# Optimization experiments

Measured on AMD Instinct MI355X. Metric: run time of the kernel, lower is better.

The kernel has to match this reference:

```python
import jax, jax.numpy as jnp
import numpy as np

B, C, H, W = 4, 64, 64, 64
RC, RS = 8, 4  # channel reduction, spatial reduction
CR = C // RC
KS = 2 * RS - 1  # 7


def _conv(x, w, b, stride, pad):
    y = jax.lax.conv_general_dilated(
        x, w, (stride, stride), [(pad, pad), (pad, pad)],
        dimension_numbers=('NCHW', 'OIHW', 'NCHW'))
    return y + b[None, :, None, None]


def setup_inputs() -> dict:
    key = jax.random.key(0)
    ks = jax.random.split(key, 13)

    def w_init(k, shape):
        fan_in = shape[1] * shape[2] * shape[3]
        return jax.random.normal(k, shape, jnp.float32) / jnp.sqrt(fan_in)

    x = jax.random.normal(ks[0], (B, C, H, W), jnp.float32)
    return {
        'x': x,
        'w1': w_init(ks[1], (CR, C, 1, 1)), 'b1': jnp.zeros((CR,), jnp.float32),
        'w2': w_init(ks[2], (CR, C, 1, 1)), 'b2': jnp.zeros((CR,), jnp.float32),
        'w3': w_init(ks[3], (C, C, 1, 1)),  'b3': jnp.zeros((C,), jnp.float32),
        'w4': w_init(ks[4], (C, C, KS, KS)), 'b4': jnp.zeros((C,), jnp.float32),
        'w5': w_init(ks[5], (C, C, KS, KS)), 'b5': jnp.zeros((C,), jnp.float32),
        'w6': w_init(ks[6], (C, C, 1, 1)),  'b6': jnp.zeros((C,), jnp.float32),
    }


def reference(x, w1, b1, w2, b2, w3, b3, w4, b4, w5, b5, w6, b6):
    gamma = 1.0
    x_ori = x
    b, c, h, w = x.shape
    n = h * w

    # ---- Block 1: spatial self-attention (SAGAN-style), N x N scores ----
    f = _conv(x, w1, b1, 1, 0).reshape(b, CR, n)   # [B, C/8, N]
    g = _conv(x, w2, b2, 1, 0).reshape(b, CR, n)   # [B, C/8, N]
    hh = _conv(x, w3, b3, 1, 0).reshape(b, c, n)   # [B, C, N]
    s = jnp.einsum('bci,bcj->bij', f, g)           # [B, N, N] = f^T g
    beta = jax.nn.softmax(s, axis=1)               # softmax over dim 1 (as in torch)
    o = jnp.einsum('bcn,bnm->bcm', hh, beta)       # [B, C, N]
    x2 = o.reshape(b, c, h, w)

    # ---- Block 2: channel attention over strided-conv features, C x C scores ----
    hp, wp = h // RS, w // RS
    npix = hp * wp
    f2 = _conv(x2, w4, b4, RS, RS - 1).reshape(b, c, npix)  # [B, C, N']
    g2 = _conv(x2, w5, b5, RS, RS - 1).reshape(b, c, npix)  # [B, C, N']
    h2 = _conv(x2, w6, b6, 1, 0).reshape(b, c, n)           # [B, C, N]
    s2 = jnp.einsum('bcn,bdn->bcd', f2, g2)                 # [B, C, C] = f g^T
    beta2 = jax.nn.softmax(s2, axis=1)
    # o[b,d,n] = sum_c h2[b,c,n] * beta2[b,c,d]
    o2 = jnp.einsum('bcn,bcd->bdn', h2, beta2).reshape(b, c, h, w)

    return gamma * o2 + x_ori
```

## Files before the change

kernel.cpp:

```cpp
#include <hip/hip_runtime.h>
#include <math.h>

#define BB 4
#define CC 64
#define CRR 8
#define NN 4096

typedef __attribute__((ext_vector_type(8))) short bf16x8;
typedef __attribute__((ext_vector_type(4))) float f32x4;

__device__ inline float bf2f(ushort u) {
    union { uint i; float f; } v; v.i = (uint)u << 16; return v.f;
}
__device__ inline ushort f2bf(float f) {
    uint u = __builtin_bit_cast(uint, f);
    u = (u + 0x7FFFu + ((u >> 16) & 1u)) >> 16;
    return (ushort)u;
}
__device__ inline uint bfpack2(float a, float b) {
    uint ua = __builtin_bit_cast(uint, a);
    uint ub = __builtin_bit_cast(uint, b);
    ua = (ua + 0x7FFFu + ((ua >> 16) & 1u)) >> 16;
    ub = (ub + 0x7FFFu + ((ub >> 16) & 1u)) & 0xFFFF0000u;
    return ua | ub;
}
__device__ inline uint pkrtz(float a, float b) {
    return __builtin_amdgcn_perm(__builtin_bit_cast(uint, b),
                                 __builtin_bit_cast(uint, a), 0x07060302u);
}
__device__ inline float fexp2(float x) {
#if __has_builtin(__builtin_amdgcn_exp2f)
    return __builtin_amdgcn_exp2f(x);
#else
    float r; asm("v_exp_f32 %0, %1" : "=v"(r) : "v"(x)); return r;
#endif
}

#define X2P_B 313600

__global__ __launch_bounds__(256) void produce_fgh(
    const float* __restrict__ x,
    const float* __restrict__ w1, const float* __restrict__ b1,
    const float* __restrict__ w2, const float* __restrict__ b2,
    const float* __restrict__ w3, const float* __restrict__ b3,
    ushort* __restrict__ fT, ushort* __restrict__ gT, ushort* __restrict__ hhb)
{
    const float LOG2E = 1.4426950408889634f;
    int t = threadIdx.x;
    int b = blockIdx.x & 3;
    int n = ((blockIdx.x >> 2) << 6) + (t & 63);
    int og = __builtin_amdgcn_readfirstlane(t >> 6);

    const float* xb = x + ((size_t)b << 18) + n;
    float xv[64];
#pragma unroll
    for (int c = 0; c < 64; ++c) xv[c] = xb[(size_t)c << 12];

    if (og == 0) {
        ushort fo[8], go[8];
#pragma unroll
        for (int k = 0; k < 8; ++k) {
            float a1 = b1[k], a2 = b2[k];
#pragma unroll
            for (int c = 0; c < 64; ++c) {
                a1 = fmaf(w1[k * 64 + c], xv[c], a1);
                a2 = fmaf(w2[k * 64 + c], xv[c], a2);
            }
            fo[k] = f2bf(a1 * LOG2E); go[k] = f2bf(a2);
        }
        uint4 fq = make_uint4((uint)fo[0] | ((uint)fo[1] << 16),
                              (uint)fo[2] | ((uint)fo[3] << 16),
                              (uint)fo[4] | ((uint)fo[5] << 16),
                              (uint)fo[6] | ((uint)fo[7] << 16));
        uint4 gq = make_uint4((uint)go[0] | ((uint)go[1] << 16),
                              (uint)go[2] | ((uint)go[3] << 16),
                              (uint)go[4] | ((uint)go[5] << 16),
                              (uint)go[6] | ((uint)go[7] << 16));
        *(uint4*)&fT[((size_t)b << 15) + (size_t)n * 8] = fq;
        *(uint4*)&gT[((size_t)b << 15) + (size_t)n * 8] = gq;
#pragma unroll
        for (int k = 0; k < 4; ++k) {
            float a = b3[k];
#pragma unroll
            for (int c = 0; c < 64; ++c) a = fmaf(w3[k * 64 + c], xv[c], a);
            hhb[((size_t)b << 18) + ((size_t)k << 12) + n] = f2bf(a);
        }
    } else {
        int c0 = og * 20 - 16;
#pragma unroll
        for (int k = 0; k < 20; ++k) {
            float a = b3[c0 + k];
#pragma unroll
            for (int c = 0; c < 64; ++c) a = fmaf(w3[(c0 + k) * 64 + c], xv[c], a);
            hhb[((size_t)b << 18) + ((size_t)(c0 + k) << 12) + n] = f2bf(a);
        }
    }
}

__global__ __launch_bounds__(256) void wtz_kernel(
    const float* __restrict__ w4, const float* __restrict__ w5,
    const float* __restrict__ w6,
    ushort* __restrict__ Wt, ushort* __restrict__ w6b, ushort* __restrict__ x2p)
{
    int bid = blockIdx.x;
    int t = threadIdx.x;
    if (bid < 128) {
        int conv = bid >> 6, co = bid & 63;
        const float* W = conv ? w5 : w4;
        for (int i = t; i < 3136; i += 256) {
            int ci = i / 49, kk = i - ci * 49;
            Wt[(((size_t)(conv * 64 + co)) * 49 + kk) * 64 + ci] = f2bf(W[co * 3136 + i]);
        }
    } else if (bid == 128) {
#pragma unroll
        for (int k = 0; k < 16; ++k) {
            int i = k * 256 + t;
            w6b[i] = f2bf(w6[i]);
        }
    } else {
        int gid = (bid - 129) * 256 + t;
        if (gid >= 4 * 804) return;
        int b = gid / 804;
        int i = gid - b * 804;
        int py, px;
        if (i < 210) { py = i / 70; px = i - py * 70; }
        else if (i < 420) { int j = i - 210; int r = j / 70; py = 67 + r; px = j - r * 70; }
        else { int j = i - 420; int r = j / 6; py = 3 + r; int c = j - r * 6; px = c < 3 ? c : 64 + c; }
        ushort* p = x2p + (size_t)b * X2P_B + (size_t)(py * 70 + px) * 64;
        uint4 z = make_uint4(0, 0, 0, 0);
#pragma unroll
        for (int k = 0; k < 8; ++k) *(uint4*)(p + k * 8) = z;
    }
}

__global__ __launch_bounds__(1024) void attn_kernel(
    const ushort* __restrict__ fT, const ushort* __restrict__ gT,
    const ushort* __restrict__ hhb, const ushort* __restrict__ w6b,
    const float* __restrict__ b6,
    ushort* __restrict__ x2p, ushort* __restrict__ h2b)
{
    __shared__ __align__(16) char smem[98304];
    ushort* hhT = (ushort*)smem;
    ushort* PstB = (ushort*)(smem + 65536);
    float* Acc = (float*)smem;
    float* Lq  = (float*)(smem + 69632);
    ushort* x2s = (ushort*)(smem + 70656);

    int t = threadIdx.x;
    int q = t >> 8, tq = t & 255;
    int l = t & 63;
    int wq = tq >> 6;
    int w16 = t >> 6;
    int ml = l & 15, g = l >> 4;
    int b = blockIdx.x & 3;
    int mt = blockIdx.x >> 2;
    int m0 = mt << 6;
    int col = m0 + wq * 16 + ml;

    const ushort* fTb = fT + ((size_t)b << 15) + (size_t)q * 8192;
    const ushort* gTb = gT + ((size_t)b << 15);
    const ushort* hhB = hhb + ((size_t)b << 18) + (q << 10);

    const bf16x8 z8 = {0, 0, 0, 0, 0, 0, 0, 0};
    const f32x4 z4 = {0.f, 0.f, 0.f, 0.f};

    bf16x8 gfrag = *(const bf16x8*)(gTb + (size_t)col * 8);
    if (g != 0) gfrag = z8;

    int sc = tq >> 2, sp = tq & 3;
    const ushort* hrowBase = hhB + (size_t)sc * 4096 + sp * 16;
    int hdst = q * 8192 + sp * 1024 + sc * 8;

    uint4 h0 = *(const uint4*)(hrowBase);
    uint4 h1 = *(const uint4*)(hrowBase + 8);
    *(uint4*)&hhT[hdst] = h0;
    *(uint4*)&hhT[hdst + 512] = h1;
    bf16x8 afc[4];
#pragma unroll
    for (int s = 0; s < 4; ++s)
        afc[s] = *(const bf16x8*)(fTb + (size_t)(16 * s + ml) * 8);

    f32x4 acc[4] = {z4, z4, z4, z4};
    float rsum = 0.f;
    int swz = (ml & 7) << 4;
    char* pbase = (char*)PstB + w16 * 2048;
    __syncthreads();

    for (int nt = 0; nt < 16; ++nt) {
        int buf = nt & 1;
        bf16x8 afn[4];
        if (nt < 15) {
            int n0 = (nt + 1) << 6;
            h0 = *(const uint4*)(hrowBase + n0);
            h1 = *(const uint4*)(hrowBase + n0 + 8);
#pragma unroll
            for (int s = 0; s < 4; ++s)
                afn[s] = *(const bf16x8*)(fTb + (size_t)(n0 + 16 * s + ml) * 8);
        }

        f32x4 Sv[4];
#pragma unroll
        for (int s = 0; s < 4; ++s)
            Sv[s] = __builtin_amdgcn_mfma_f32_16x16x32_bf16(afc[s], gfrag, z4, 0, 0, 0);

        uint plo[4], phi[4];
#pragma unroll
        for (int s = 0; s < 4; ++s) {
            float p0 = fexp2(Sv[s][0]);
            float p1 = fexp2(Sv[s][1]);
            float p2 = fexp2(Sv[s][2]);
            float p3 = fexp2(Sv[s][3]);
            rsum += (p0 + p1) + (p2 + p3);
            plo[s] = pkrtz(p0, p1);
            phi[s] = pkrtz(p2, p3);
        }

#pragma unroll
        for (int s = 0; s < 4; ++s) {
            uint off = (uint)((ml * 128 + 32 * s + 8 * g) ^ swz);
            *(uint2*)(pbase + off) = make_uint2(plo[s], phi[s]);
        }

#pragma unroll
        for (int kk = 0; kk < 2; ++kk) {
            uint off = (uint)((ml * 128 + 64 * kk + 16 * g) ^ swz);
            bf16x8 pf = *(const bf16x8*)(pbase + off);
#pragma unroll
            for (int ct = 0; ct < 4; ++ct) {
                bf16x8 hf = *(const bf16x8*)&hhT[q * 8192 + buf * 4096 + (kk * 4 + g) * 512 + (16 * ct + ml) * 8];
                acc[ct] = __builtin_amdgcn_mfma_f32_16x16x32_bf16(hf, pf, acc[ct], 0, 0, 0);
            }
        }

        if (nt < 15) {
            int nb = (nt + 1) & 1;
            *(uint4*)&hhT[hdst + nb * 4096] = h0;
            *(uint4*)&hhT[hdst + nb * 4096 + 512] = h1;
#pragma unroll
            for (int s = 0; s < 4; ++s) afc[s] = afn[s];
        }
        __syncthreads();
    }

    rsum += __shfl_xor(rsum, 16);
    rsum += __shfl_xor(rsum, 32);

    {
        float* arow = Acc + q * 4352 + (wq * 16 + ml) * 68;
#pragma unroll
        for (int ct = 0; ct < 4; ++ct)
            *(f32x4*)(arow + 16 * ct + 4 * g) = acc[ct];
        if (g == 0) Lq[q * 64 + wq * 16 + ml] = rsum;
    }
    __syncthreads();

    {
        int m = t >> 4, c0 = (t & 15) << 2;
        float Ltot = Lq[m] + Lq[64 + m] + Lq[128 + m] + Lq[192 + m];
        float rL = 1.f / Ltot;
        f32x4 v0 = *(const f32x4*)(Acc + 0 * 4352 + m * 68 + c0);
        f32x4 v1 = *(const f32x4*)(Acc + 1 * 4352 + m * 68 + c0);
        f32x4 v2 = *(const f32x4*)(Acc + 2 * 4352 + m * 68 + c0);
        f32x4 v3 = *(const f32x4*)(Acc + 3 * 4352 + m * 68 + c0);
        f32x4 v;
#pragma unroll
        for (int r = 0; r < 4; ++r)
            v[r] = ((v0[r] + v1[r]) + (v2[r] + v3[r])) * rL;
        uint2 pk = make_uint2(bfpack2(v[0], v[1]), bfpack2(v[2], v[3]));
        int px = m + 3, py = mt + 3;
        *(uint2*)(x2p + (size_t)b * X2P_B + (size_t)(py * 70 + px) * 64 + c0) = pk;
        *(uint2*)(x2s + m * 72 + c0) = pk;
    }
    __syncthreads();

    {
        int dt = w16 & 3, mq = w16 >> 2;
        f32x4 hacc = z4;
#pragma unroll
        for (int kk = 0; kk < 2; ++kk) {
            bf16x8 xf = *(const bf16x8*)(x2s + (mq * 16 + ml) * 72 + 32 * kk + 8 * g);
            bf16x8 wf = *(const bf16x8*)(w6b + (size_t)(16 * dt + ml) * 64 + 32 * kk + 8 * g);
            hacc = __builtin_amdgcn_mfma_f32_16x16x32_bf16(wf, xf, hacc, 0, 0, 0);
        }
        ushort* h2row = h2b + ((size_t)b << 18) + (m0 + mq * 16 + ml);
#pragma unroll
        for (int r = 0; r < 4; ++r) {
            int d = 16 * dt + 4 * g + r;
            h2row[(size_t)d << 12] = f2bf(hacc[r] + b6[d]);
        }
    }
}

__global__ __launch_bounds__(448) void conv7_kernel(
    const ushort* __restrict__ x2p, const ushort* __restrict__ Wt,
    const float* __restrict__ b4, const float* __restrict__ b5,
    float* __restrict__ f2, float* __restrict__ g2)
{
    __shared__ float red[7][512];
    int t = threadIdx.x;
    int l = t & 63, ky = t >> 6;
    int ml = l & 15, g = l >> 4;
    int bid = blockIdx.x;
    int bc = bid & 7;
    int sub = bid >> 3;
    int ct = sub & 3, oh = sub >> 2;
    int conv = bc & 1, b = bc >> 1;

    int co0 = ct * 16;
    const ushort* wb = Wt + (size_t)conv * 200704
                     + (size_t)(co0 + ml) * 3136 + (size_t)(ky * 7) * 64 + g * 8;
    const ushort* xbase = x2p + (size_t)b * X2P_B + g * 8;

    int pixoff[2];
#pragma unroll
    for (int s = 0; s < 2; ++s) {
        int opix = oh * 32 + s * 16 + ml;
        int oy = opix >> 4, ox = opix & 15;
        pixoff[s] = ((oy * 4 + ky) * 70 + ox * 4) * 64;
    }

    const f32x4 z4 = {0.f, 0.f, 0.f, 0.f};
    f32x4 acc[2] = {z4, z4};

#pragma unroll
    for (int kx = 0; kx < 7; ++kx) {
#pragma unroll
        for (int ci0 = 0; ci0 < 64; ci0 += 32) {
            bf16x8 av = *(const bf16x8*)(wb + kx * 64 + ci0);
#pragma unroll
            for (int s = 0; s < 2; ++s) {
                bf16x8 bv = *(const bf16x8*)(xbase + pixoff[s] + kx * 64 + ci0);
                acc[s] = __builtin_amdgcn_mfma_f32_16x16x32_bf16(av, bv, acc[s], 0, 0, 0);
            }
        }
    }

#pragma unroll
    for (int s = 0; s < 2; ++s)
#pragma unroll
        for (int r = 0; r < 4; ++r)
            red[ky][(4 * g + r) * 32 + s * 16 + ml] = acc[s][r];
    __syncthreads();

    const float* bias = conv ? b5 : b4;
    float* y = conv ? g2 : f2;
    for (int idx = t; idx < 512; idx += 448) {
        float s = red[0][idx];
        s += red[1][idx]; s += red[2][idx]; s += red[3][idx];
        s += red[4][idx]; s += red[5][idx]; s += red[6][idx];
        int co = co0 + (idx >> 5);
        int opix = oh * 32 + (idx & 31);
        y[((size_t)(b * 64 + co) << 8) + opix] = s + bias[co];
    }
}

__global__ __launch_bounds__(1024) void s2_softmax_kernel(
    const float* __restrict__ f2, const float* __restrict__ g2,
    float* __restrict__ beta2)
{
    __shared__ __align__(16) float g2t[4][64][68];
    __shared__ __align__(16) float s2f[64][68];
    __shared__ float red[6][64];
    int t = threadIdx.x;
    int b = blockIdx.x;
    int q = t >> 8, tq = t & 255;
    int nb = q * 64;

    {
        int n = tq & 63, c0 = tq >> 6;
#pragma unroll
        for (int k = 0; k < 16; ++k) {
            int cc = c0 * 16 + k;
            g2t[q][n][cc] = g2[((size_t)(b * 64 + cc) << 8) + nb + n];
        }
    }
    __syncthreads();

    int c = tq & 63, dq = tq >> 6, d0 = dq * 16;
    float acc[16];
#pragma unroll
    for (int k = 0; k < 16; ++k) acc[k] = 0.f;
    const float* frow = f2 + ((size_t)(b * 64 + c) << 8) + nb;
#pragma unroll 4
    for (int n = 0; n < 64; ++n) {
        float fv = frow[n];
#pragma unroll
        for (int jj = 0; jj < 4; ++jj) {
            float4 gv = *(const float4*)&g2t[q][n][d0 + jj * 4];
            acc[jj * 4 + 0] = fmaf(fv, gv.x, acc[jj * 4 + 0]);
            acc[jj * 4 + 1] = fmaf(fv, gv.y, acc[jj * 4 + 1]);
            acc[jj * 4 + 2] = fmaf(fv, gv.z, acc[jj * 4 + 2]);
            acc[jj * 4 + 3] = fmaf(fv, gv.w, acc[jj * 4 + 3]);
        }
    }
    __syncthreads();
    float* part = &g2t[0][0][0];
#pragma unroll
    for (int k = 0; k < 16; ++k) part[q * 4096 + c * 64 + d0 + k] = acc[k];
    __syncthreads();
    {
        int idx = t * 4;
        int cc = idx >> 6, dd = idx & 63;
        float4 s0 = *(const float4*)&part[cc * 64 + dd];
        float4 s1 = *(const float4*)&part[4096 + cc * 64 + dd];
        float4 s2v = *(const float4*)&part[8192 + cc * 64 + dd];
        float4 s3 = *(const float4*)&part[12288 + cc * 64 + dd];
        float4 s;
        s.x = (s0.x + s1.x) + (s2v.x + s3.x);
        s.y = (s0.y + s1.y) + (s2v.y + s3.y);
        s.z = (s0.z + s1.z) + (s2v.z + s3.z);
        s.w = (s0.w + s1.w) + (s2v.w + s3.w);
        *(float4*)&s2f[cc][dd] = s;
    }
    __syncthreads();
    if (t < 256) {
        int d = t & 63, cq = t >> 6;
        float mx = -3e38f;
#pragma unroll
        for (int k = 0; k < 16; ++k) mx = fmaxf(mx, s2f[cq * 16 + k][d]);
        red[cq][d] = mx;
    }
    __syncthreads();
    if (t < 64)
        red[4][t] = fmaxf(fmaxf(red[0][t], red[1][t]), fmaxf(red[2][t], red[3][t]));
    __syncthreads();
    if (t < 256) {
        int d = t & 63, cq = t >> 6;
        float mx = red[4][d];
        float s = 0.f;
#pragma unroll
        for (int k = 0; k < 16; ++k) s += __expf(s2f[cq * 16 + k][d] - mx);
        red[cq][d] = s;
    }
    __syncthreads();
    if (t < 64)
        red[5][t] = 1.f / ((red[0][t] + red[1][t]) + (red[2][t] + red[3][t]));
    __syncthreads();
    if (t < 256) {
        int d = t & 63, cq = t >> 6;
        float mx = red[4][d], r = red[5][d];
#pragma unroll
        for (int k = 0; k < 16; ++k) {
            int cc = cq * 16 + k;
            beta2[((size_t)b << 12) + cc * 64 + d] = __expf(s2f[cc][d] - mx) * r;
        }
    }
}

__global__ __launch_bounds__(256) void o2_residual_kernel(
    const ushort* __restrict__ h2b, const float* __restrict__ beta2,
    const float* __restrict__ x, float* __restrict__ out)
{
    __shared__ __align__(16) float b2s[64][64];
    __shared__ float h2s[64][65];
    int t = threadIdx.x;
    int b = blockIdx.x & 3;
    int n0 = (blockIdx.x >> 2) << 6;

    {
#pragma unroll
        for (int k = 0; k < 16; ++k) {
            int idx = k * 256 + t;
            b2s[idx >> 6][idx & 63] = beta2[((size_t)b << 12) + idx];
        }
        int n = t & 63; int c0 = t >> 6;
#pragma unroll
        for (int k = 0; k < 16; ++k) {
            int cc = c0 * 16 + k;
            h2s[cc][n] = bf2f(h2b[((size_t)(b * 64 + cc) << 12) + n0 + n]);
        }
    }
    __syncthreads();

    int n = t & 63, dg = t >> 6, d0 = dg * 16;
    float acc[16];
#pragma unroll
    for (int k = 0; k < 16; ++k) acc[k] = 0.f;

    for (int cc = 0; cc < 64; ++cc) {
        float hv = h2s[cc][n];
#pragma unroll
        for (int jj = 0; jj < 4; ++jj) {
            float4 bv = *reinterpret_cast<const float4*>(&b2s[cc][d0 + jj * 4]);
            acc[jj * 4 + 0] = fmaf(hv, bv.x, acc[jj * 4 + 0]);
            acc[jj * 4 + 1] = fmaf(hv, bv.y, acc[jj * 4 + 1]);
            acc[jj * 4 + 2] = fmaf(hv, bv.z, acc[jj * 4 + 2]);
            acc[jj * 4 + 3] = fmaf(hv, bv.w, acc[jj * 4 + 3]);
        }
    }
#pragma unroll
    for (int k = 0; k < 16; ++k) {
        int d = d0 + k;
        size_t o = ((size_t)(b * 64 + d) << 12) + n0 + n;
        out[o] = acc[k] + x[o];
    }
}

extern "C" void kernel_launch(void* const* d_in, const int* in_sizes, int n_in,
                              void* d_out, int out_size, void* d_ws, size_t ws_size,
                              hipStream_t stream)
{
    const float* x  = (const float*)d_in[0];
    const float* w1 = (const float*)d_in[1];
    const float* b1 = (const float*)d_in[2];
    const float* w2 = (const float*)d_in[3];
    const float* b2 = (const float*)d_in[4];
    const float* w3 = (const float*)d_in[5];
    const float* b3 = (const float*)d_in[6];
    const float* w4 = (const float*)d_in[7];
    const float* b4 = (const float*)d_in[8];
    const float* w5 = (const float*)d_in[9];
    const float* b5 = (const float*)d_in[10];
    const float* w6 = (const float*)d_in[11];
    const float* b6 = (const float*)d_in[12];
    float* out = (float*)d_out;

    ushort* u = (ushort*)d_ws;
    ushort* fT  = u;
    ushort* gT  = fT + 131072;
    ushort* hhb = gT + 131072;
    ushort* x2p = hhb + 1048576;
    ushort* h2b = x2p + 1254400;
    ushort* Wt  = h2b + 1048576;
    ushort* w6b = Wt + 401408;
    float* fr    = (float*)(w6b + 4096);
    float* f2    = fr;
    float* g2    = fr + 65536;
    float* beta2 = fr + 131072;

    produce_fgh<<<256, 256, 0, stream>>>(x, w1, b1, w2, b2, w3, b3, fT, gT, hhb);
    wtz_kernel<<<142, 256, 0, stream>>>(w4, w5, w6, Wt, w6b, x2p);
    attn_kernel<<<256, 1024, 0, stream>>>(fT, gT, hhb, w6b, b6, x2p, h2b);
    conv7_kernel<<<256, 448, 0, stream>>>(x2p, Wt, b4, b5, f2, g2);
    s2_softmax_kernel<<<BB, 1024, 0, stream>>>(f2, g2, beta2);
    o2_residual_kernel<<<256, 256, 0, stream>>>(h2b, beta2, x, out);
}
```

Before: 79.80 us.

## Split channel-score softmax across more blocks and use MFMA for output mix

The channel-attention score/softmax kernel used to run as 4 blocks of 1024 threads, one per batch. It now runs as 64 blocks, each computing four output columns, so more compute units take part. The output-mixing kernel moves from scalar FP32 FMAs to bf16 MFMA, splitting beta2 into high and low bf16 parts to keep accuracy. In exchange, f2 is read redundantly by every block and the split-bf16 product can lose some precision.

```diff
diff --git a/kernel.cpp b/kernel.cpp
--- a/kernel.cpp
+++ b/kernel.cpp
@@ -354,96 +354,80 @@
     }
 }
 
-__global__ __launch_bounds__(1024) void s2_softmax_kernel(
+__global__ __launch_bounds__(256) void s2_softmax_kernel(
     const float* __restrict__ f2, const float* __restrict__ g2,
     float* __restrict__ beta2)
 {
-    __shared__ __align__(16) float g2t[4][64][68];
-    __shared__ __align__(16) float s2f[64][68];
-    __shared__ float red[6][64];
+    __shared__ __align__(16) float g2t[256][8];
+    __shared__ __align__(16) float part[16][64][4];
+    __shared__ __align__(16) float s2f[64][4];
+    __shared__ float mx4[4], rs4[4];
     int t = threadIdx.x;
-    int b = blockIdx.x;
-    int q = t >> 8, tq = t & 255;
-    int nb = q * 64;
+    int b = blockIdx.x & 3;
+    int d0 = (blockIdx.x >> 2) << 2;
 
     {
-        int n = tq & 63, c0 = tq >> 6;
-#pragma unroll
-        for (int k = 0; k < 16; ++k) {
-            int cc = c0 * 16 + k;
-            g2t[q][n][cc] = g2[((size_t)(b * 64 + cc) << 8) + nb + n];
-        }
-    }
-    __syncthreads();
-
-    int c = tq & 63, dq = tq >> 6, d0 = dq * 16;
-    float acc[16];
-#pragma unroll
-    for (int k = 0; k < 16; ++k) acc[k] = 0.f;
-    const float* frow = f2 + ((size_t)(b * 64 + c) << 8) + nb;
+        int dd = t & 3, n0 = (t >> 2) << 2;
+        const float* gp = g2 + ((size_t)(b * 64 + d0 + dd) << 8) + n0;
+        float4 v = *(const float4*)gp;
+        g2t[n0 + 0][dd] = v.x; g2t[n0 + 1][dd] = v.y;
+        g2t[n0 + 2][dd] = v.z; g2t[n0 + 3][dd] = v.w;
+    }
+    __syncthreads();
+
+    int c0 = (t & 15) << 2, nq = t >> 4;
+    float acc[4][4];
+#pragma unroll
+    for (int i = 0; i < 4; ++i)
+#pragma unroll
+        for (int j = 0; j < 4; ++j) acc[i][j] = 0.f;
+    const float* fb = f2 + ((size_t)(b * 64) << 8);
 #pragma unroll 4
-    for (int n = 0; n < 64; ++n) {
-        float fv = frow[n];
-#pragma unroll
-        for (int jj = 0; jj < 4; ++jj) {
-            float4 gv = *(const float4*)&g2t[q][n][d0 + jj * 4];
-            acc[jj * 4 + 0] = fmaf(fv, gv.x, acc[jj * 4 + 0]);
-            acc[jj * 4 + 1] = fmaf(fv, gv.y, acc[jj * 4 + 1]);
-            acc[jj * 4 + 2] = fmaf(fv, gv.z, acc[jj * 4 + 2]);
-            acc[jj * 4 + 3] = fmaf(fv, gv.w, acc[jj * 4 + 3]);
-        }
-    }
-    __syncthreads();
-    float* part = &g2t[0][0][0];
-#pragma unroll
-    for (int k = 0; k < 16; ++k) part[q * 4096 + c * 64 + d0 + k] = acc[k];
+    for (int i = 0; i < 16; ++i) {
+        int n = (nq << 4) + ((i + nq) & 15);
+        float4 gv = *(const float4*)&g2t[n][0];
+        float fv0 = fb[(c0 + 0) * 256 + n];
+        float fv1 = fb[(c0 + 1) * 256 + n];
+        float fv2 = fb[(c0 + 2) * 256 + n];
+        float fv3 = fb[(c0 + 3) * 256 + n];
+        acc[0][0] = fmaf(fv0, gv.x, acc[0][0]); acc[0][1] = fmaf(fv0, gv.y, acc[0][1]);
+        acc[0][2] = fmaf(fv0, gv.z, acc[0][2]); acc[0][3] = fmaf(fv0, gv.w, acc[0][3]);
+        acc[1][0] = fmaf(fv1, gv.x, acc[1][0]); acc[1][1] = fmaf(fv1, gv.y, acc[1][1]);
+        acc[1][2] = fmaf(fv1, gv.z, acc[1][2]); acc[1][3] = fmaf(fv1, gv.w, acc[1][3]);
+        acc[2][0] = fmaf(fv2, gv.x, acc[2][0]); acc[2][1] = fmaf(fv2, gv.y, acc[2][1]);
+        acc[2][2] = fmaf(fv2, gv.z, acc[2][2]); acc[2][3] = fmaf(fv2, gv.w, acc[2][3]);
+        acc[3][0] = fmaf(fv3, gv.x, acc[3][0]); acc[3][1] = fmaf(fv3, gv.y, acc[3][1]);
+        acc[3][2] = fmaf(fv3, gv.z, acc[3][2]); acc[3][3] = fmaf(fv3, gv.w, acc[3][3]);
+    }
+#pragma unroll
+    for (int i = 0; i < 4; ++i)
+        *(float4*)&part[nq][c0 + i][0] =
+            make_float4(acc[i][0], acc[i][1], acc[i][2], acc[i][3]);
+    __syncthreads();
+
+    if (t < 64) {
+        int c = t;
+        float4 s = make_float4(0.f, 0.f, 0.f, 0.f);
+#pragma unroll
+        for (int q2 = 0; q2 < 16; ++q2) {
+            float4 v = *(const float4*)&part[q2][c][0];
+            s.x += v.x; s.y += v.y; s.z += v.z; s.w += v.w;
+        }
+        *(float4*)&s2f[c][0] = s;
+    }
+    __syncthreads();
+    if (t < 4) {
+        float mxv = s2f[0][t];
+        for (int c = 1; c < 64; ++c) mxv = fmaxf(mxv, s2f[c][t]);
+        float sm = 0.f;
+        for (int c = 0; c < 64; ++c) sm += __expf(s2f[c][t] - mxv);
+        mx4[t] = mxv; rs4[t] = 1.f / sm;
+    }
     __syncthreads();
     {
-        int idx = t * 4;
-        int cc = idx >> 6, dd = idx & 63;
-        float4 s0 = *(const float4*)&part[cc * 64 + dd];
-        float4 s1 = *(const float4*)&part[4096 + cc * 64 + dd];
-        float4 s2v = *(const float4*)&part[8192 + cc * 64 + dd];
-        float4 s3 = *(const float4*)&part[12288 + cc * 64 + dd];
-        float4 s;
-        s.x = (s0.x + s1.x) + (s2v.x + s3.x);
-        s.y = (s0.y + s1.y) + (s2v.y + s3.y);
-        s.z = (s0.z + s1.z) + (s2v.z + s3.z);
-        s.w = (s0.w + s1.w) + (s2v.w + s3.w);
-        *(float4*)&s2f[cc][dd] = s;
-    }
-    __syncthreads();
-    if (t < 256) {
-        int d = t & 63, cq = t >> 6;
-        float mx = -3e38f;
-#pragma unroll
-        for (int k = 0; k < 16; ++k) mx = fmaxf(mx, s2f[cq * 16 + k][d]);
-        red[cq][d] = mx;
-    }
-    __syncthreads();
-    if (t < 64)
-        red[4][t] = fmaxf(fmaxf(red[0][t], red[1][t]), fmaxf(red[2][t], red[3][t]));
-    __syncthreads();
-    if (t < 256) {
-        int d = t & 63, cq = t >> 6;
-        float mx = red[4][d];
-        float s = 0.f;
-#pragma unroll
-        for (int k = 0; k < 16; ++k) s += __expf(s2f[cq * 16 + k][d] - mx);
-        red[cq][d] = s;
-    }
-    __syncthreads();
-    if (t < 64)
-        red[5][t] = 1.f / ((red[0][t] + red[1][t]) + (red[2][t] + red[3][t]));
-    __syncthreads();
-    if (t < 256) {
-        int d = t & 63, cq = t >> 6;
-        float mx = red[4][d], r = red[5][d];
-#pragma unroll
-        for (int k = 0; k < 16; ++k) {
-            int cc = cq * 16 + k;
-            beta2[((size_t)b << 12) + cc * 64 + d] = __expf(s2f[cc][d] - mx) * r;
-        }
+        int c = t >> 2, dd = t & 3;
+        beta2[((size_t)b << 12) + c * 64 + d0 + dd] =
+            __expf(s2f[c][dd] - mx4[dd]) * rs4[dd];
     }
 }
 
@@ -451,49 +435,63 @@
     const ushort* __restrict__ h2b, const float* __restrict__ beta2,
     const float* __restrict__ x, float* __restrict__ out)
 {
-    __shared__ __align__(16) float b2s[64][64];
-    __shared__ float h2s[64][65];
+    __shared__ __align__(16) ushort bt[64][68];
+    __shared__ __align__(16) ushort btl[64][68];
+    __shared__ __align__(16) ushort hn[64][68];
     int t = threadIdx.x;
     int b = blockIdx.x & 3;
     int n0 = (blockIdx.x >> 2) << 6;
+    int l = t & 63, w = t >> 6;
+    int ml = l & 15, g = l >> 4;
 
     {
-#pragma unroll
-        for (int k = 0; k < 16; ++k) {
-            int idx = k * 256 + t;
-            b2s[idx >> 6][idx & 63] = beta2[((size_t)b << 12) + idx];
-        }
-        int n = t & 63; int c0 = t >> 6;
-#pragma unroll
-        for (int k = 0; k < 16; ++k) {
-            int cc = c0 * 16 + k;
-            h2s[cc][n] = bf2f(h2b[((size_t)(b * 64 + cc) << 12) + n0 + n]);
-        }
-    }
-    __syncthreads();
-
-    int n = t & 63, dg = t >> 6, d0 = dg * 16;
-    float acc[16];
-#pragma unroll
-    for (int k = 0; k < 16; ++k) acc[k] = 0.f;
-
-    for (int cc = 0; cc < 64; ++cc) {
-        float hv = h2s[cc][n];
-#pragma unroll
-        for (int jj = 0; jj < 4; ++jj) {
-            float4 bv = *reinterpret_cast<const float4*>(&b2s[cc][d0 + jj * 4]);
-            acc[jj * 4 + 0] = fmaf(hv, bv.x, acc[jj * 4 + 0]);
-            acc[jj * 4 + 1] = fmaf(hv, bv.y, acc[jj * 4 + 1]);
-            acc[jj * 4 + 2] = fmaf(hv, bv.z, acc[jj * 4 + 2]);
-            acc[jj * 4 + 3] = fmaf(hv, bv.w, acc[jj * 4 + 3]);
-        }
-    }
-#pragma unroll
-    for (int k = 0; k < 16; ++k) {
-        int d = d0 + k;
-        size_t o = ((size_t)(b * 64 + d) << 12) + n0 + n;
-        out[o] = acc[k] + x[o];
-    }
+        int c = t >> 2, o16 = (t & 3) << 4;
+        const float* bp = beta2 + ((size_t)b << 12) + c * 64 + o16;
+#pragma unroll
+        for (int i = 0; i < 16; i += 4) {
+            float4 v = *(const float4*)(bp + i);
+            float vv[4] = {v.x, v.y, v.z, v.w};
+#pragma unroll
+            for (int k = 0; k < 4; ++k) {
+                ushort hi = f2bf(vv[k]);
+                bt[o16 + i + k][c] = hi;
+                btl[o16 + i + k][c] = f2bf(vv[k] - bf2f(hi));
+            }
+        }
+        const ushort* hp = h2b + ((size_t)(b * 64 + c) << 12) + n0 + o16;
+#pragma unroll
+        for (int i = 0; i < 16; i += 8) {
+            uint4 hv = *(const uint4*)(hp + i);
+            const ushort* hs = (const ushort*)&hv;
+#pragma unroll
+            for (int k = 0; k < 8; ++k) hn[o16 + i + k][c] = hs[k];
+        }
+    }
+    __syncthreads();
+
+    const f32x4 z4 = {0.f, 0.f, 0.f, 0.f};
+    f32x4 acc[4] = {z4, z4, z4, z4};
+#pragma unroll
+    for (int kk = 0; kk < 2; ++kk) {
+        bf16x8 ah = *(const bf16x8*)&bt[w * 16 + ml][kk * 32 + g * 8];
+        bf16x8 al = *(const bf16x8*)&btl[w * 16 + ml][kk * 32 + g * 8];
+#pragma unroll
+        for (int nt = 0; nt < 4; ++nt) {
+            bf16x8 bv = *(const bf16x8*)&hn[nt * 16 + ml][kk * 32 + g * 8];
+            acc[nt] = __builtin_amdgcn_mfma_f32_16x16x32_bf16(ah, bv, acc[nt], 0, 0, 0);
+            acc[nt] = __builtin_amdgcn_mfma_f32_16x16x32_bf16(al, bv, acc[nt], 0, 0, 0);
+        }
+    }
+
+#pragma unroll
+    for (int nt = 0; nt < 4; ++nt)
+#pragma unroll
+        for (int r = 0; r < 4; ++r) {
+            int d = w * 16 + g * 4 + r;
+            int n = n0 + nt * 16 + ml;
+            size_t o = ((size_t)(b * 64 + d) << 12) + n;
+            out[o] = acc[nt][r] + x[o];
+        }
 }
 
 extern "C" void kernel_launch(void* const* d_in, const int* in_sizes, int n_in,
@@ -532,6 +530,6 @@
     wtz_kernel<<<142, 256, 0, stream>>>(w4, w5, w6, Wt, w6b, x2p);
     attn_kernel<<<256, 1024, 0, stream>>>(fT, gT, hhb, w6b, b6, x2p, h2b);
     conv7_kernel<<<256, 448, 0, stream>>>(x2p, Wt, b4, b5, f2, g2);
-    s2_softmax_kernel<<<BB, 1024, 0, stream>>>(f2, g2, beta2);
+    s2_softmax_kernel<<<64, 256, 0, stream>>>(f2, g2, beta2);
     o2_residual_kernel<<<256, 256, 0, stream>>>(h2b, beta2, x, out);
 }
```

Result: faster. 75.44 us, median of 2 (-5.5%).
